# Kernel tuning notes

Measured on AMD Instinct MI355X. Metric: run time of the kernel, lower is better.

Reference implementation:

```python
import jax, jax.numpy as jnp
import numpy as np

B, S, C = 4, 2048, 2048
D = C // 4  # head dim = 512

def setup_inputs() -> dict:
    key = jax.random.key(0)
    k1, k2, k3, k4, k5 = jax.random.split(key, 5)
    scale = 1.0 / np.sqrt(C)
    return {
        "x": jax.random.normal(k1, (B, S, C), dtype=jnp.float32),
        "Wqkv": jax.random.normal(k2, (3 * D, C), dtype=jnp.float32) * scale,
        "bqkv": jax.random.normal(k3, (3 * D,), dtype=jnp.float32) * 0.01,
        "Wo": jax.random.normal(k4, (C, D), dtype=jnp.float32) * (1.0 / np.sqrt(D)),
        "bo": jax.random.normal(k5, (C,), dtype=jnp.float32) * 0.01,
    }

def reference(x, Wqkv, bqkv, Wo, bo):
    Bx, Sx, Cx = x.shape
    d = Cx // 4
    # fused QKV projection: [B,S,3d] -> split into q,k,v each [B,S,d]
    qkv = jnp.einsum('bsc,oc->bso', x, Wqkv) + bqkv
    qkv = qkv.reshape(Bx, Sx, 3, d)
    q, k, v = qkv[:, :, 0], qkv[:, :, 1], qkv[:, :, 2]
    # scaled dot-product attention (full [B,S,S] scores, as in original)
    attn = jnp.einsum('bqd,bkd->bqk', q, k) / jnp.sqrt(jnp.asarray(d, x.dtype))
    attn = jax.nn.softmax(attn, axis=-1)
    ctx = jnp.einsum('bqk,bkd->bqd', attn, v)
    # output projection d -> C
    return jnp.einsum('bsd,od->bso', ctx, Wo) + bo
```

## Files before the change

### kernel.cpp

```cpp
#include <hip/hip_runtime.h>
#include <math.h>


typedef __bf16 bf16;
typedef bf16 bf16x8 __attribute__((ext_vector_type(8)));
typedef bf16 bf16x4 __attribute__((ext_vector_type(4)));
typedef float f32x4 __attribute__((ext_vector_type(4)));

#define BB 4
#define SS 2048
#define CC 2048
#define DD 512
#define ND3 1536
#define MM 8192

typedef const __attribute__((address_space(1))) unsigned int g_u32;
typedef __attribute__((address_space(3))) unsigned int l_u32;

__device__ __forceinline__ void gl_lds16(const bf16* g, bf16* l) {
    __builtin_amdgcn_global_load_lds((g_u32*)g, (l_u32*)l, 16, 0, 0);
}

#define N4_X   (MM * CC / 4)
#define N4_WQ  (ND3 * CC / 4)
#define N4_WO  (CC * DD / 4)
#define N4_RS  (MM / 4)
#define N4_TOT (N4_X + N4_WQ + N4_WO + N4_RS)

__global__ __launch_bounds__(256) void prep(const float* __restrict__ x,
                                            const float* __restrict__ Wqkv,
                                            const float* __restrict__ Wo,
                                            bf16* __restrict__ xb,
                                            bf16* __restrict__ wqkvb,
                                            bf16* __restrict__ wob,
                                            float* __restrict__ rsum) {
    int i = blockIdx.x * 256 + threadIdx.x;
    const int stride = gridDim.x * 256;
    for (; i < N4_TOT; i += stride) {
        if (i < N4_X + N4_WQ + N4_WO) {
            const float* src; bf16* dst; int j = i;
            if (j < N4_X)                { src = x;    dst = xb; }
            else if (j < N4_X + N4_WQ)   { src = Wqkv; dst = wqkvb; j -= N4_X; }
            else                         { src = Wo;   dst = wob;   j -= N4_X + N4_WQ; }
            float4 v = ((const float4*)src)[j];
            bf16x4 o;
            o[0] = (bf16)v.x; o[1] = (bf16)v.y; o[2] = (bf16)v.z; o[3] = (bf16)v.w;
            ((bf16x4*)dst)[j] = o;
        } else {
            int j = i - (N4_X + N4_WQ + N4_WO);
            ((float4*)rsum)[j] = float4{0.f, 0.f, 0.f, 0.f};
        }
    }
}

template <bool OUT_BF16, int BN, int EPI>
__global__ __launch_bounds__(256) void gemm_bt(const bf16* __restrict__ A,
                                               const bf16* __restrict__ Bm,
                                               const float* __restrict__ bias,
                                               float* __restrict__ rowsum,
                                               bf16* __restrict__ vTp,
                                               void* __restrict__ Cv,
                                               int K, int lda, int ldb, int ldc,
                                               long ab, long bb, long cb,
                                               float scale) {
    constexpr int TM = (BN == 128) ? 4 : 2;
    __shared__ bf16 As[128 * 32];
    __shared__ bf16 Bs[BN * 32];
    A += (size_t)blockIdx.z * ab;
    Bm += (size_t)blockIdx.z * bb;
    const int m0 = blockIdx.y * 128, n0 = blockIdx.x * BN;
    const int t = threadIdx.x, lane = t & 63, w = t >> 6;
    const int wm = (BN == 128) ? (w >> 1) * 64 : w * 32;
    const int wn = (BN == 128) ? (w & 1) * 64 : 0;
    const int q = lane >> 4, cl = lane & 15;
    const int srow = lane >> 2;
    const int scol = (lane & 3) * 8;
    const bf16* pa0 = A + (size_t)(m0 + w * 16 + srow) * lda + scol;
    const bf16* pa1 = pa0 + (size_t)64 * lda;
    const bf16* pb0 = Bm + (size_t)(n0 + w * 16 + srow) * ldb + scol;
    const bf16* pb1 = pb0 + (size_t)64 * ldb;
    bf16* lA0 = As + (w * 16) * 32;
    bf16* lA1 = As + (64 + w * 16) * 32;
    bf16* lB0 = Bs + (w * 16) * 32;
    bf16* lB1 = Bs + (64 + w * 16) * 32;

    f32x4 acc[TM][4] = {};
    for (int k0 = 0; k0 < K; k0 += 32) {
        gl_lds16(pa0 + k0, lA0);
        gl_lds16(pa1 + k0, lA1);
        gl_lds16(pb0 + k0, lB0);
        if constexpr (BN == 128) gl_lds16(pb1 + k0, lB1);
        __syncthreads();
        bf16x8 af[TM], bfr[4];
#pragma unroll
        for (int i = 0; i < TM; i++)
            af[i] = *(const bf16x8*)&As[(wm + i * 16 + cl) * 32 + q * 8];
#pragma unroll
        for (int j = 0; j < 4; j++)
            bfr[j] = *(const bf16x8*)&Bs[(wn + j * 16 + cl) * 32 + q * 8];
#pragma unroll
        for (int i = 0; i < TM; i++)
#pragma unroll
            for (int j = 0; j < 4; j++)
                acc[i][j] = __builtin_amdgcn_mfma_f32_16x16x32_bf16(af[i], bfr[j], acc[i][j], 0, 0, 0);
        __syncthreads();
    }

    if constexpr (EPI == 4 || EPI == 5) {
        float inv[4], cs[4] = {0.f, 0.f, 0.f, 0.f};
        if constexpr (EPI == 5) {
#pragma unroll
            for (int j = 0; j < 4; j++)
                inv[j] = 1.0f / rowsum[(size_t)blockIdx.z * SS + n0 + wn + j * 16 + cl];
        }
#pragma unroll
        for (int i = 0; i < TM; i++)
#pragma unroll
            for (int j = 0; j < 4; j++) {
                int col = n0 + wn + j * 16 + cl;
                int row = m0 + wm + i * 16 + q * 4;
                bf16x4 o;
                if constexpr (EPI == 4) {
#pragma unroll
                    for (int r = 0; r < 4; r++) {
                        float e = __expf(acc[i][j][r] * scale);
                        cs[j] += e;
                        o[r] = (bf16)e;
                    }
                } else {
#pragma unroll
                    for (int r = 0; r < 4; r++) o[r] = (bf16)(acc[i][j][r] * inv[j]);
                }
                *(bf16x4*)&((bf16*)Cv)[(size_t)blockIdx.z * cb + (size_t)col * ldc + row] = o;
            }
        if constexpr (EPI == 4) {
#pragma unroll
            for (int j = 0; j < 4; j++) {
                cs[j] += __shfl_xor(cs[j], 16, 64);
                cs[j] += __shfl_xor(cs[j], 32, 64);
            }
            if (q == 0) {
#pragma unroll
                for (int j = 0; j < 4; j++)
                    atomicAdd(&rowsum[(size_t)blockIdx.z * SS + n0 + wn + j * 16 + cl], cs[j]);
            }
        }
        return;
    }

    const bool v_block = (EPI == 3) && (n0 >= 1024);
#pragma unroll
    for (int i = 0; i < TM; i++) {
#pragma unroll
        for (int j = 0; j < 4; j++) {
            int col = n0 + wn + j * 16 + cl;
            float bvv = bias ? bias[col] : 0.0f;
            if (v_block) {
                int row = m0 + wm + i * 16 + q * 4;
                int b = row >> 11, s = row & 2047;
                bf16x4 o;
#pragma unroll
                for (int r = 0; r < 4; r++) o[r] = (bf16)(acc[i][j][r] * scale + bvv);
                *(bf16x4*)&vTp[((size_t)b * DD + (col - 1024)) * SS + s] = o;
            } else {
#pragma unroll
                for (int r = 0; r < 4; r++) {
                    int row = m0 + wm + i * 16 + q * 4 + r;
                    float val = acc[i][j][r] * scale + bvv;
                    if (OUT_BF16)
                        ((bf16*)Cv)[(size_t)blockIdx.z * cb + (size_t)row * ldc + col] = (bf16)val;
                    else
                        ((float*)Cv)[(size_t)blockIdx.z * cb + (size_t)row * ldc + col] = val;
                }
            }
        }
    }
}

extern "C" void kernel_launch(void* const* d_in, const int* in_sizes, int n_in,
                              void* d_out, int out_size, void* d_ws, size_t ws_size,
                              hipStream_t stream) {
    const float* x    = (const float*)d_in[0];
    const float* Wqkv = (const float*)d_in[1];
    const float* bqkv = (const float*)d_in[2];
    const float* Wo   = (const float*)d_in[3];
    const float* bo   = (const float*)d_in[4];
    float* out = (float*)d_out;

    char* ws = (char*)d_ws;
    size_t off = 0;
    bf16* xb    = (bf16*)(ws + off); off += (size_t)MM * CC * 2;
    bf16* wqkvb = (bf16*)(ws + off); off += (size_t)ND3 * CC * 2;
    bf16* wob   = (bf16*)(ws + off); off += (size_t)CC * DD * 2;
    bf16* qkvb  = (bf16*)(ws + off); off += (size_t)MM * ND3 * 2;
    bf16* vT    = (bf16*)(ws + off); off += (size_t)BB * DD * SS * 2;
    bf16* expS  = (bf16*)(ws + off); off += (size_t)BB * SS * SS * 2;
    bf16* ctxb  = (bf16*)(ws + off); off += (size_t)MM * DD * 2;
    float* rsum = (float*)(ws + off); off += (size_t)MM * 4;

    prep<<<2048, 256, 0, stream>>>(x, Wqkv, Wo, xb, wqkvb, wob, rsum);

    gemm_bt<true, 128, 3><<<dim3(ND3 / 128, MM / 128, 1), 256, 0, stream>>>(
        xb, wqkvb, bqkv, nullptr, vT, qkvb, CC, CC, CC, ND3, 0, 0, 0, 1.0f);

    gemm_bt<true, 128, 4><<<dim3(SS / 128, SS / 128, BB), 256, 0, stream>>>(
        qkvb + 512 , qkvb , nullptr, rsum, nullptr, expS,
        DD, ND3, ND3, SS,
        (long)SS * ND3, (long)SS * ND3, (long)SS * SS,
        0.044194173824159216f );

    gemm_bt<true, 64, 5><<<dim3(SS / 64, DD / 128, BB), 256, 0, stream>>>(
        vT, expS, nullptr, rsum, nullptr, ctxb,
        SS, SS, SS, DD,
        (long)DD * SS, (long)SS * SS, (long)SS * DD, 1.0f);

    gemm_bt<false, 128, 0><<<dim3(CC / 128, MM / 128, 1), 256, 0, stream>>>(
        ctxb, wob, bo, nullptr, nullptr, out, DD, DD, DD, CC, 0, 0, 0, 1.0f);

    (void)in_sizes; (void)n_in; (void)out_size; (void)ws_size;
}
```

Before: 332.0 us.

## Double K-tile to 64 with XOR-swizzled LDS layout in GEMM kernels

The shared GEMM body now loads a 64-wide K slice per iteration instead of 32. That halves the number of barrier pairs per K loop and doubles the MFMA work between syncs. The LDS tile uses an XOR swizzle of 16-byte blocks by row, both on the async global-to-LDS store and on the fragment read, to avoid bank conflicts on the wider rows. The kernel is split into thin named wrappers per epilogue, and LDS use per block doubles, which may reduce occupancy.

```diff
diff --git a/kernel.cpp b/kernel.cpp
--- a/kernel.cpp
+++ b/kernel.cpp
@@ -54,18 +54,19 @@
 }
 
 template <bool OUT_BF16, int BN, int EPI>
-__global__ __launch_bounds__(256) void gemm_bt(const bf16* __restrict__ A,
-                                               const bf16* __restrict__ Bm,
-                                               const float* __restrict__ bias,
-                                               float* __restrict__ rowsum,
-                                               bf16* __restrict__ vTp,
-                                               void* __restrict__ Cv,
-                                               int K, int lda, int ldb, int ldc,
-                                               long ab, long bb, long cb,
-                                               float scale) {
+__device__ __forceinline__ void gemm_body(const bf16* __restrict__ A,
+                                          const bf16* __restrict__ Bm,
+                                          const float* __restrict__ bias,
+                                          float* __restrict__ rowsum,
+                                          bf16* __restrict__ vTp,
+                                          void* __restrict__ Cv,
+                                          int K, int lda, int ldb, int ldc,
+                                          long ab, long bb, long cb,
+                                          float scale) {
     constexpr int TM = (BN == 128) ? 4 : 2;
-    __shared__ bf16 As[128 * 32];
-    __shared__ bf16 Bs[BN * 32];
+    constexpr int NB = (BN == 128) ? 4 : 2;
+    __shared__ bf16 As[128 * 64];
+    __shared__ bf16 Bs[BN * 64];
     A += (size_t)blockIdx.z * ab;
     Bm += (size_t)blockIdx.z * bb;
     const int m0 = blockIdx.y * 128, n0 = blockIdx.x * BN;
@@ -73,36 +74,42 @@
     const int wm = (BN == 128) ? (w >> 1) * 64 : w * 32;
     const int wn = (BN == 128) ? (w & 1) * 64 : 0;
     const int q = lane >> 4, cl = lane & 15;
-    const int srow = lane >> 2;
-    const int scol = (lane & 3) * 8;
-    const bf16* pa0 = A + (size_t)(m0 + w * 16 + srow) * lda + scol;
-    const bf16* pa1 = pa0 + (size_t)64 * lda;
-    const bf16* pb0 = Bm + (size_t)(n0 + w * 16 + srow) * ldb + scol;
-    const bf16* pb1 = pb0 + (size_t)64 * ldb;
-    bf16* lA0 = As + (w * 16) * 32;
-    bf16* lA1 = As + (64 + w * 16) * 32;
-    bf16* lB0 = Bs + (w * 16) * 32;
-    bf16* lB1 = Bs + (64 + w * 16) * 32;
+    const int srow = lane >> 3;
+    const int sblk = (lane & 7) ^ srow;
+    const int scol = sblk * 8;
+    const bf16* pa = A + (size_t)(m0 + w * 32 + srow) * lda + scol;
+    const int brow0 = (BN == 128) ? w * 32 : w * 16;
+    const bf16* pb = Bm + (size_t)(n0 + brow0 + srow) * ldb + scol;
+    bf16* lA = As + (w * 32) * 64;
+    bf16* lB = Bs + brow0 * 64;
+    const int rblk0 = (q ^ (cl & 7)) * 8;
+    const int rblk1 = ((4 + q) ^ (cl & 7)) * 8;
 
     f32x4 acc[TM][4] = {};
-    for (int k0 = 0; k0 < K; k0 += 32) {
-        gl_lds16(pa0 + k0, lA0);
-        gl_lds16(pa1 + k0, lA1);
-        gl_lds16(pb0 + k0, lB0);
-        if constexpr (BN == 128) gl_lds16(pb1 + k0, lB1);
+    for (int k0 = 0; k0 < K; k0 += 64) {
+#pragma unroll
+        for (int n = 0; n < 4; n++)
+            gl_lds16(pa + k0 + (size_t)(n * 8) * lda, lA + n * 8 * 64);
+#pragma unroll
+        for (int n = 0; n < NB; n++)
+            gl_lds16(pb + k0 + (size_t)(n * 8) * ldb, lB + n * 8 * 64);
         __syncthreads();
-        bf16x8 af[TM], bfr[4];
-#pragma unroll
-        for (int i = 0; i < TM; i++)
-            af[i] = *(const bf16x8*)&As[(wm + i * 16 + cl) * 32 + q * 8];
-#pragma unroll
-        for (int j = 0; j < 4; j++)
-            bfr[j] = *(const bf16x8*)&Bs[(wn + j * 16 + cl) * 32 + q * 8];
-#pragma unroll
-        for (int i = 0; i < TM; i++)
+#pragma unroll
+        for (int h = 0; h < 2; h++) {
+            const int rb = h ? rblk1 : rblk0;
+            bf16x8 af[TM], bfr[4];
+#pragma unroll
+            for (int i = 0; i < TM; i++)
+                af[i] = *(const bf16x8*)&As[(wm + i * 16 + cl) * 64 + rb];
 #pragma unroll
             for (int j = 0; j < 4; j++)
-                acc[i][j] = __builtin_amdgcn_mfma_f32_16x16x32_bf16(af[i], bfr[j], acc[i][j], 0, 0, 0);
+                bfr[j] = *(const bf16x8*)&Bs[(wn + j * 16 + cl) * 64 + rb];
+#pragma unroll
+            for (int i = 0; i < TM; i++)
+#pragma unroll
+                for (int j = 0; j < 4; j++)
+                    acc[i][j] = __builtin_amdgcn_mfma_f32_16x16x32_bf16(af[i], bfr[j], acc[i][j], 0, 0, 0);
+        }
         __syncthreads();
     }
 
@@ -175,6 +182,27 @@
             }
         }
     }
+}
+
+__global__ __launch_bounds__(256) void k_qkv(const bf16* A, const bf16* Bm,
+        const float* bias, bf16* vTp, void* Cv, int K, int lda, int ldb, int ldc,
+        float scale) {
+    gemm_body<true, 128, 3>(A, Bm, bias, nullptr, vTp, Cv, K, lda, ldb, ldc, 0, 0, 0, scale);
+}
+__global__ __launch_bounds__(256) void k_score(const bf16* A, const bf16* Bm,
+        float* rowsum, void* Cv, int K, int lda, int ldb, int ldc,
+        long ab, long bb, long cb, float scale) {
+    gemm_body<true, 128, 4>(A, Bm, nullptr, rowsum, nullptr, Cv, K, lda, ldb, ldc, ab, bb, cb, scale);
+}
+__global__ __launch_bounds__(256) void k_pv(const bf16* A, const bf16* Bm,
+        float* rowsum, void* Cv, int K, int lda, int ldb, int ldc,
+        long ab, long bb, long cb, float scale) {
+    gemm_body<true, 64, 5>(A, Bm, nullptr, rowsum, nullptr, Cv, K, lda, ldb, ldc, ab, bb, cb, scale);
+}
+__global__ __launch_bounds__(256) void k_out(const bf16* A, const bf16* Bm,
+        const float* bias, void* Cv, int K, int lda, int ldb, int ldc,
+        float scale) {
+    gemm_body<false, 128, 0>(A, Bm, bias, nullptr, nullptr, Cv, K, lda, ldb, ldc, 0, 0, 0, scale);
 }
 
 extern "C" void kernel_launch(void* const* d_in, const int* in_sizes, int n_in,
@@ -200,22 +228,22 @@
 
     prep<<<2048, 256, 0, stream>>>(x, Wqkv, Wo, xb, wqkvb, wob, rsum);
 
-    gemm_bt<true, 128, 3><<<dim3(ND3 / 128, MM / 128, 1), 256, 0, stream>>>(
-        xb, wqkvb, bqkv, nullptr, vT, qkvb, CC, CC, CC, ND3, 0, 0, 0, 1.0f);
-
-    gemm_bt<true, 128, 4><<<dim3(SS / 128, SS / 128, BB), 256, 0, stream>>>(
-        qkvb + 512 , qkvb , nullptr, rsum, nullptr, expS,
+    k_qkv<<<dim3(ND3 / 128, MM / 128, 1), 256, 0, stream>>>(
+        xb, wqkvb, bqkv, vT, qkvb, CC, CC, CC, ND3, 1.0f);
+
+    k_score<<<dim3(SS / 128, SS / 128, BB), 256, 0, stream>>>(
+        qkvb + 512 , qkvb , rsum, expS,
         DD, ND3, ND3, SS,
         (long)SS * ND3, (long)SS * ND3, (long)SS * SS,
         0.044194173824159216f );
 
-    gemm_bt<true, 64, 5><<<dim3(SS / 64, DD / 128, BB), 256, 0, stream>>>(
-        vT, expS, nullptr, rsum, nullptr, ctxb,
+    k_pv<<<dim3(SS / 64, DD / 128, BB), 256, 0, stream>>>(
+        vT, expS, rsum, ctxb,
         SS, SS, SS, DD,
         (long)DD * SS, (long)SS * SS, (long)SS * DD, 1.0f);
 
-    gemm_bt<false, 128, 0><<<dim3(CC / 128, MM / 128, 1), 256, 0, stream>>>(
-        ctxb, wob, bo, nullptr, nullptr, out, DD, DD, DD, CC, 0, 0, 0, 1.0f);
+    k_out<<<dim3(CC / 128, MM / 128, 1), 256, 0, stream>>>(
+        ctxb, wob, bo, out, DD, DD, DD, CC, 1.0f);
 
     (void)in_sizes; (void)n_in; (void)out_size; (void)ws_size;
 }
```

Result: faster. 302.7 us (-8.8%).
